# Performance work log

Measured on AMD Instinct MI355X. Metric: run time of the kernel, lower is better.

Reference implementation:

```python
import math
import jax, jax.numpy as jnp
import numpy as np

B, N, D_FULL, M, D_V = 8, 4096, 256, 256, 256


def _phi(x, omega):
    # x: [..., N, d_full], omega: [M, d_full] -> [..., N, M]
    proj = x @ omega.T
    log_phi = proj - 0.5 * jnp.sum(x * x, axis=-1, keepdims=True)
    log_phi = log_phi - jnp.max(log_phi, axis=-1, keepdims=True)
    return jnp.exp(log_phi) / math.sqrt(omega.shape[0])


def _causal(phi_q, phi_k, V):
    # phi_q/phi_k: [B, N, M], V: [B, N, d_v]
    b, n, m = phi_q.shape
    d_v = V.shape[-1]

    def step(carry, inp):
        S, z = carry
        pq, pk, v = inp  # [B,M], [B,M], [B,d_v]
        S = S + pk[:, :, None] * v[:, None, :]          # [B, M, d_v]
        z = z + pk                                       # [B, M]
        num = jnp.einsum('bi,bij->bj', pq, S)            # [B, d_v]
        den = jnp.maximum(jnp.sum(pq * z, axis=-1), 1e-6)
        return (S, z), num / den[:, None]

    S0 = jnp.zeros((b, m, d_v), phi_q.dtype)
    z0 = jnp.zeros((b, m), phi_q.dtype)
    xs = (jnp.swapaxes(phi_q, 0, 1), jnp.swapaxes(phi_k, 0, 1), jnp.swapaxes(V, 0, 1))
    _, ys = jax.lax.scan(step, (S0, z0), xs)  # ys: [N, B, d_v]
    return jnp.swapaxes(ys, 0, 1)


def setup_inputs() -> dict:
    key = jax.random.key(0)
    kq, kk, kv, ko = jax.random.split(key, 4)
    Q = jax.random.normal(kq, (B, N, D_FULL), dtype=jnp.float32)
    K_in = jax.random.normal(kk, (B, N, D_FULL), dtype=jnp.float32)
    V = jax.random.normal(kv, (B, N, D_V), dtype=jnp.float32)
    omega = jax.random.normal(ko, (M, D_FULL), dtype=jnp.float32)
    return {"Q": Q, "K_in": K_in, "V": V, "omega": omega, "causal": 1}


def reference(Q, K_in, V, omega, causal):
    phi_q = _phi(Q, omega)
    phi_k = _phi(K_in, omega)
    if causal:
        return _causal(phi_q, phi_k, V)
    S = jnp.einsum('bni,bnj->bij', phi_k, V)          # [B, M, d_v]
    z = jnp.sum(phi_k, axis=-2)                        # [B, M]
    num = jnp.einsum('bni,bij->bnj', phi_q, S)
    den = jnp.maximum(jnp.einsum('bni,bi->bn', phi_q, z), 1e-6)
    return num / den[..., None]
```

## Files before the change

### kernel.cpp

```cpp
#include <hip/hip_runtime.h>

#define BN 8
#define NN 4096
#define DD 256
#define MM 256
#define DV 256
#define CHUNK 256
#define NC (NN / CHUNK)

using f32x4 = __attribute__((ext_vector_type(4))) float;
using s16x8 = __attribute__((ext_vector_type(8))) short;

#define MFMA16(a, b, c) __builtin_amdgcn_mfma_f32_16x16x32_bf16(a, b, c, 0, 0, 0)


__device__ __forceinline__ unsigned short f2bf(float x) {
    union { float f; unsigned int u; } v; v.f = x;
    unsigned int r = v.u + 0x7FFF + ((v.u >> 16) & 1);
    return (unsigned short)(r >> 16);
}
__device__ __forceinline__ float bf2f(unsigned short u) {
    union { unsigned int u; float f; } v; v.u = ((unsigned int)u) << 16;
    return v.f;
}

__device__ __forceinline__ void split4(const float4 x, unsigned short h[4], unsigned short l[4])
{
    const float xs[4] = {x.x, x.y, x.z, x.w};
#pragma unroll
    for (int j = 0; j < 4; ++j) {
        union { float f; unsigned u; } v; v.f = xs[j];
        const unsigned hm = v.u & 0xFFFF0000u;
        union { unsigned u; float f; } hv; hv.u = hm;
        h[j] = (unsigned short)(hm >> 16);
        l[j] = f2bf(xs[j] - hv.f);
    }
}

__global__ __launch_bounds__(256) void omconv(
    const float* __restrict__ Om, unsigned short* __restrict__ OmH,
    unsigned short* __restrict__ OmL)
{
    const int i = blockIdx.x * 256 + threadIdx.x;
    const int row = i >> 6;
    const int k0  = (i & 63) * 4;
    const float4 v = *(const float4*)(Om + (size_t)row * DD + k0);
    const int wv = row >> 6, ct = (row >> 4) & 3, colL = row & 15;
    const int kt = k0 >> 5, quad = (k0 >> 3) & 3, e0 = k0 & 7;
    const int lanep = quad * 16 + colL;
    const size_t off = ((size_t)((wv * 8 + kt) * 4 + ct) * 64 + lanep) * 8 + e0;
    unsigned short h[4], l[4];
    split4(v, h, l);
    *(uint2*)(OmH + off) = *(uint2*)h;
    *(uint2*)(OmL + off) = *(uint2*)l;
}

__global__ __launch_bounds__(256, 4) void phi_fused(
    const float* __restrict__ Qp, const float* __restrict__ Kp,
    const unsigned short* __restrict__ OmH, const unsigned short* __restrict__ OmL,
    unsigned short* __restrict__ PhiQ, unsigned short* __restrict__ PhiKF,
    unsigned short* __restrict__ PhiTF, float* __restrict__ Zp)
{
    const int tid = threadIdx.x;
    const int w = tid >> 6;
    const int lane = tid & 63;
    const int col = lane & 15, quad = lane >> 4;
    const bool kpath = blockIdx.x < 1024;
    const int id = kpath ? blockIdx.x : (blockIdx.x - 1024);
    const float* __restrict__ X = kpath ? Kp : Qp;
    const long r0 = (long)id * 32;

    __shared__ __align__(16) short AhS[32][264];
    __shared__ __align__(16) short AlS[32][264];
    __shared__ float rowmax_s[32];
    float (*red)[68] = (float(*)[68])AhS;
    unsigned short (*P)[264] = (unsigned short(*)[264])AlS;
    unsigned int* P32 = (unsigned int*)AlS;

    {
        float4 xv[8];
#pragma unroll
        for (int j = 0; j < 8; ++j) {
            const int row = w * 8 + j;
            xv[j] = *(const float4*)(X + (r0 + row) * DD + lane * 4);
        }
#pragma unroll
        for (int j = 0; j < 8; ++j) {
            const int row = w * 8 + j;
            unsigned short h[4], l[4];
            split4(xv[j], h, l);
            *(uint2*)&AhS[row][lane * 4] = *(uint2*)h;
            *(uint2*)&AlS[row][lane * 4] = *(uint2*)l;
        }
    }

    const unsigned short* OmHw = OmH + (size_t)w * 8 * 4 * 512;
    const unsigned short* OmLw = OmL + (size_t)w * 8 * 4 * 512;
    f32x4 acc[2][4] = {};
    s16x8 bh0[4], bl0[4], bh1[4], bl1[4];
#pragma unroll
    for (int ct = 0; ct < 4; ++ct) {
        const size_t off = ((size_t)ct * 64 + lane) * 8;
        bh0[ct] = *(const s16x8*)(OmHw + off);
        bl0[ct] = *(const s16x8*)(OmLw + off);
    }
    __syncthreads();

#pragma unroll
    for (int kt = 0; kt < 8; ++kt) {
        if (kt < 7) {
#pragma unroll
            for (int ct = 0; ct < 4; ++ct) {
                const size_t off = ((size_t)((kt + 1) * 4 + ct) * 64 + lane) * 8;
                bh1[ct] = *(const s16x8*)(OmHw + off);
                bl1[ct] = *(const s16x8*)(OmLw + off);
            }
        }
#pragma unroll
        for (int t = 0; t < 2; ++t) {
            const s16x8 ah = *(const s16x8*)&AhS[t * 16 + col][kt * 32 + quad * 8];
            const s16x8 al = *(const s16x8*)&AlS[t * 16 + col][kt * 32 + quad * 8];
#pragma unroll
            for (int ct = 0; ct < 4; ++ct) {
                acc[t][ct] = MFMA16(ah, bh0[ct], acc[t][ct]);
                acc[t][ct] = MFMA16(ah, bl0[ct], acc[t][ct]);
                acc[t][ct] = MFMA16(al, bh0[ct], acc[t][ct]);
            }
        }
#pragma unroll
        for (int ct = 0; ct < 4; ++ct) { bh0[ct] = bh1[ct]; bl0[ct] = bl1[ct]; }
    }

    __syncthreads();
#pragma unroll
    for (int t = 0; t < 2; ++t)
#pragma unroll
        for (int r = 0; r < 4; ++r) {
            float m = acc[t][0][r];
#pragma unroll
            for (int ct = 1; ct < 4; ++ct) m = fmaxf(m, acc[t][ct][r]);
            red[t * 16 + quad * 4 + r][w * 16 + col] = m;
        }
    __syncthreads();
    {
        const int row = tid >> 3, seg = tid & 7;
        float m = red[row][seg * 8];
#pragma unroll
        for (int j = 1; j < 8; ++j) m = fmaxf(m, red[row][seg * 8 + j]);
        m = fmaxf(m, __shfl_xor(m, 1));
        m = fmaxf(m, __shfl_xor(m, 2));
        m = fmaxf(m, __shfl_xor(m, 4));
        if (seg == 0) rowmax_s[row] = m;
    }
    __syncthreads();

#pragma unroll
    for (int t = 0; t < 2; ++t)
#pragma unroll
        for (int r = 0; r < 4; ++r) {
            const int n = t * 16 + quad * 4 + r;
            const float rm = rowmax_s[n];
#pragma unroll
            for (int ct = 0; ct < 4; ++ct) {
                const float val = __expf(acc[t][ct][r] - rm) * 0.0625f;
                const unsigned u = (unsigned)f2bf(val);
                const unsigned up = (unsigned)__shfl_xor((int)u, 1);
                if ((col & 1) == 0)
                    P32[n * 132 + w * 32 + ct * 8 + (col >> 1)] = u | (up << 16);
            }
        }
    __syncthreads();

    if (!kpath) {
        const int t7 = tid & 7;
        const int nb = tid >> 3;
#pragma unroll
        for (int s = 0; s < 4; ++s)
            *(uint4*)(PhiQ + (r0 + nb) * MM + t7 * 8 + s * 64) =
                *(const uint4*)&P[nb][t7 * 8 + s * 64];
    } else {
        const int b = id >> 7;
        const int ib = id & 127;
        const int c = ib >> 3;
        const size_t bc = ((size_t)(b * NC + c)) << 16;
        const int jt = (ib >> 1) & 3;
        const int half = ib & 1;
        const int ktp = ib & 7;
#pragma unroll
        for (int p = 0; p < 4; ++p) {
            const int msw = p * 4 + (tid >> 6);
            const int ms = msw >> 1, wl = msw & 1;
            const uint4 v = *(const uint4*)&P[wl * 16 + (lane & 15)][ms * 32 + (lane >> 4) * 8];
            *(uint4*)(PhiKF + bc + (((size_t)(jt * 8 + ms) * 4 + half * 2 + wl) * 64 + lane) * 8) = v;
        }
#pragma unroll
        for (int p = 0; p < 4; ++p) {
            const int mq = p, t = tid >> 6;
            unsigned short u[8];
#pragma unroll
            for (int e = 0; e < 8; ++e)
                u[e] = P[(lane >> 4) * 8 + e][mq * 64 + t * 16 + (lane & 15)];
            *(uint4*)(PhiTF + bc + (((size_t)(mq * 8 + ktp) * 4 + t) * 64 + lane) * 8) = *(uint4*)u;
        }
        float z = 0.f;
#pragma unroll
        for (int n = 0; n < 32; ++n) z += bf2f(P[n][tid]);
        atomicAdd(&Zp[((b * NC + c) << 8) + tid], z);
    }
}

__global__ __launch_bounds__(256) void transpose_v(
    const float* __restrict__ V, unsigned short* __restrict__ VTF)
{
    const int tid = threadIdx.x;
    const int ct = blockIdx.x & 3;
    const long r0 = (long)(blockIdx.x >> 2) * 64;
    const int b = (int)(r0 >> 12);
    const int n0 = (int)(r0 & (NN - 1));
    const int c = n0 >> 8;
    const int kt0 = (n0 & 255) >> 5;
    const size_t bc = ((size_t)(b * NC + c)) << 16;
    __shared__ unsigned short T[64][72];
    const int rr = tid >> 4, cs = tid & 15;
#pragma unroll
    for (int p = 0; p < 4; ++p) {
        const int r = p * 16 + rr;
        const float4 v = *(const float4*)(V + (r0 + r) * DV + ct * 64 + cs * 4);
        T[cs * 4 + 0][r] = f2bf(v.x); T[cs * 4 + 1][r] = f2bf(v.y);
        T[cs * 4 + 2][r] = f2bf(v.z); T[cs * 4 + 3][r] = f2bf(v.w);
    }
    __syncthreads();
    const int t = (tid >> 6) & 3, lane = tid & 63;
#pragma unroll
    for (int p = 0; p < 2; ++p) {
        const int kt2 = p;
        const uint4 v = *(const uint4*)&T[t * 16 + (lane & 15)][kt2 * 32 + (lane >> 4) * 8];
        *(uint4*)(VTF + bc + (((size_t)(ct * 8 + kt0 + kt2) * 4 + t) * 64 + lane) * 8) = v;
    }
}

__global__ __launch_bounds__(256, 3) void state_mfma(
    const unsigned short* __restrict__ VTF, const unsigned short* __restrict__ PhiTF,
    unsigned short* __restrict__ STF)
{
    const int tid = threadIdx.x;
    const int w = tid >> 6;
    const int lane = tid & 63;
    const int col = lane & 15, quad = lane >> 4;
    const int q  = blockIdx.x >> 7;
    const int bci = blockIdx.x & 127;
    const int c  = bci & 15;
    const int b  = bci >> 4;
    const int dvq = (q & 1) * 2 + (w & 1);
    const int mq  = (q >> 1) * 2 + (w >> 1);
    const size_t bc = ((size_t)(b * NC + c)) << 16;
    const unsigned short* Af = VTF   + bc + (size_t)dvq * 16384;
    const unsigned short* Bf = PhiTF + bc + (size_t)mq  * 16384;

    f32x4 acc[4][4] = {};
    s16x8 a0[4], b0[4], a1[4], b1[4];
#pragma unroll
    for (int t = 0; t < 4; ++t) {
        a0[t] = *(const s16x8*)(Af + ((size_t)t * 64 + lane) * 8);
        b0[t] = *(const s16x8*)(Bf + ((size_t)t * 64 + lane) * 8);
    }
#pragma unroll
    for (int kt = 0; kt < 8; ++kt) {
        if (kt < 7) {
#pragma unroll
            for (int t = 0; t < 4; ++t) {
                a1[t] = *(const s16x8*)(Af + ((size_t)((kt + 1) * 4 + t) * 64 + lane) * 8);
                b1[t] = *(const s16x8*)(Bf + ((size_t)((kt + 1) * 4 + t) * 64 + lane) * 8);
            }
        }
#pragma unroll
        for (int i = 0; i < 4; ++i)
#pragma unroll
            for (int j = 0; j < 4; ++j) acc[i][j] = MFMA16(b0[i], a0[j], acc[i][j]);
#pragma unroll
        for (int t = 0; t < 4; ++t) { a0[t] = a1[t]; b0[t] = b1[t]; }
    }
#pragma unroll
    for (int i = 0; i < 4; ++i)
#pragma unroll
        for (int j = 0; j < 4; ++j) {
            unsigned short s[4];
#pragma unroll
            for (int r = 0; r < 4; ++r) s[r] = f2bf(acc[i][j][r]);
            const int lanep = ((i & 1) * 2 + (quad >> 1)) * 16 + col;
            const size_t off = (((size_t)(dvq * 8 + mq * 2 + (i >> 1)) * 4 + j) * 64 + lanep) * 8 + (quad & 1) * 4;
            *(uint2*)(STF + bc + off) = *(uint2*)s;
        }
}

__global__ __launch_bounds__(256) void prefix2(
    unsigned short* __restrict__ ST, float* __restrict__ Z)
{
    const long idx = (long)blockIdx.x * 256 + threadIdx.x;
    const int b = (int)(idx >> 16);
    const int r = (int)(idx & 65535);
    float run = 0.f;
#pragma unroll
    for (int c = 0; c < NC; ++c) {
        const size_t off = (((size_t)(b * NC + c)) << 16) + r;
        const float v = bf2f(ST[off]);
        ST[off] = f2bf(run);
        run += v;
    }
    if (idx < BN * MM) {
        const int b2 = (int)(idx >> 8);
        const int m = (int)(idx & 255);
        float rz = 0.f;
#pragma unroll
        for (int c = 0; c < NC; ++c) {
            const size_t off = (size_t)(b2 * NC + c) * MM + m;
            const float v = Z[off];
            Z[off] = rz;
            rz += v;
        }
    }
}

__global__ __launch_bounds__(256) void out_mfma(
    const unsigned short* __restrict__ PhiQ, const unsigned short* __restrict__ PhiKF,
    const unsigned short* __restrict__ VTF, const unsigned short* __restrict__ STF,
    const float* __restrict__ Z, float* __restrict__ Out)
{
    const int tid = threadIdx.x;
    const int w = tid >> 6;
    const int lane = tid & 63;
    const int col = lane & 15, quad = lane >> 4;
    const int it = 3 - (blockIdx.x >> 7);
    const int low = blockIdx.x & 127;
    const int c  = low & 15;
    const int b  = low >> 4;
    const size_t chunk_row = (size_t)b * NN + (size_t)c * CHUNK;
    const size_t bc = ((size_t)(b * NC + c)) << 16;
    const unsigned short* Qrow = PhiQ + (chunk_row + it * 64) * MM;
    const unsigned short* Vf = VTF + bc + (size_t)w * 16384;
    const unsigned short* Sf = STF + bc + (size_t)w * 16384;

    __shared__ unsigned short Qs[64][264];
    __shared__ unsigned short A_s[64][72];
    __shared__ float red[64][68];
    __shared__ float z_s[256];
    __shared__ float den_s[64];

    const float zval = Z[((size_t)(b * NC + c) << 8) + tid];
    s16x8 bk0[8], bk1[8];
#pragma unroll
    for (int ms = 0; ms < 8; ++ms)
        bk0[ms] = *(const s16x8*)(PhiKF + bc + (((size_t)ms * 4 + w) * 64 + lane) * 8);
    uint4 qv[8];
#pragma unroll
    for (int i = 0; i < 8; ++i)
        qv[i] = *((const uint4*)Qrow + i * 256 + tid);
    z_s[tid] = zval;
#pragma unroll
    for (int i = 0; i < 8; ++i) {
        const int f = i * 256 + tid;
        *(uint4*)&Qs[f >> 5][(f & 31) * 8] = qv[i];
    }
    __syncthreads();

    f32x4 oacc[4][4] = {};
    float rsum[4][4] = {};

    for (int jt = 0; jt <= it; ++jt) {
        s16x8 bv[8];
#pragma unroll
        for (int ks2 = 0; ks2 < 2; ++ks2)
#pragma unroll
            for (int t2 = 0; t2 < 4; ++t2)
                bv[ks2 * 4 + t2] = *(const s16x8*)(Vf + (((size_t)(jt * 2 + ks2) * 4 + t2) * 64 + lane) * 8);
        f32x4 accA[4] = {};
#pragma unroll
        for (int ms = 0; ms < 8; ++ms)
#pragma unroll
            for (int t = 0; t < 4; ++t) {
                const s16x8 aq = *(const s16x8*)&Qs[t * 16 + col][ms * 32 + quad * 8];
                accA[t] = MFMA16(aq, bk0[ms], accA[t]);
            }
        if (jt < it) {
#pragma unroll
            for (int ms = 0; ms < 8; ++ms)
                bk1[ms] = *(const s16x8*)(PhiKF + bc + (((size_t)((jt + 1) * 8 + ms) * 4 + w) * 64 + lane) * 8);
        }
        __syncthreads();
#pragma unroll
        for (int t = 0; t < 4; ++t)
#pragma unroll
            for (int r = 0; r < 4; ++r) {
                const int i_loc = t * 16 + quad * 4 + r;
                const int j_loc = w * 16 + col;
                float v = (jt * 64 + j_loc <= it * 64 + i_loc) ? accA[t][r] : 0.f;
                rsum[t][r] += v;
                A_s[i_loc][j_loc] = f2bf(v);
            }
        __syncthreads();
#pragma unroll
        for (int ks2 = 0; ks2 < 2; ++ks2) {
            s16x8 av[4];
#pragma unroll
            for (int t = 0; t < 4; ++t)
                av[t] = *(const s16x8*)&A_s[t * 16 + col][ks2 * 32 + quad * 8];
#pragma unroll
            for (int t2 = 0; t2 < 4; ++t2)
#pragma unroll
                for (int t = 0; t < 4; ++t)
                    oacc[t][t2] = MFMA16(av[t], bv[ks2 * 4 + t2], oacc[t][t2]);
        }
#pragma unroll
        for (int ms = 0; ms < 8; ++ms) bk0[ms] = bk1[ms];
    }
#pragma unroll
    for (int t = 0; t < 4; ++t)
#pragma unroll
        for (int r = 0; r < 4; ++r)
            red[t * 16 + quad * 4 + r][w * 16 + col] = rsum[t][r];

    s16x8 bs0[4], bs1[4];
#pragma unroll
    for (int t2 = 0; t2 < 4; ++t2)
        bs0[t2] = *(const s16x8*)(Sf + ((size_t)t2 * 64 + lane) * 8);
#pragma unroll
    for (int ms = 0; ms < 8; ++ms) {
        if (ms < 7) {
#pragma unroll
            for (int t2 = 0; t2 < 4; ++t2)
                bs1[t2] = *(const s16x8*)(Sf + ((size_t)((ms + 1) * 4 + t2) * 64 + lane) * 8);
        }
        s16x8 aq[4];
#pragma unroll
        for (int t = 0; t < 4; ++t)
            aq[t] = *(const s16x8*)&Qs[t * 16 + col][ms * 32 + quad * 8];
#pragma unroll
        for (int t2 = 0; t2 < 4; ++t2)
#pragma unroll
            for (int t = 0; t < 4; ++t)
                oacc[t][t2] = MFMA16(aq[t], bs0[t2], oacc[t][t2]);
#pragma unroll
        for (int t2 = 0; t2 < 4; ++t2) bs0[t2] = bs1[t2];
    }
    {
        const int i = tid & 63;
        const int seg = tid >> 6;
        float d = 0.f;
#pragma unroll
        for (int g = 0; g < 8; ++g) {
            const s16x8 qv8 = *(const s16x8*)&Qs[i][seg * 64 + g * 8];
#pragma unroll
            for (int x = 0; x < 8; ++x)
                d = fmaf(bf2f((unsigned short)qv8[x]), z_s[seg * 64 + g * 8 + x], d);
        }
        red[i][64 + seg] = d;
    }
    __syncthreads();
    if (tid < 64) {
        float s = 0.f;
#pragma unroll
        for (int j = 0; j < 68; ++j) s += red[tid][j];
        den_s[tid] = fmaxf(s, 1e-6f);
    }
    __syncthreads();
#pragma unroll
    for (int t = 0; t < 4; ++t)
#pragma unroll
        for (int r = 0; r < 4; ++r) {
            const int i_loc = t * 16 + quad * 4 + r;
            const float invd = 1.0f / den_s[i_loc];
#pragma unroll
            for (int t2 = 0; t2 < 4; ++t2)
                Out[(chunk_row + it * 64 + i_loc) * DV + w * 64 + t2 * 16 + col] = oacc[t][t2][r] * invd;
        }
}

extern "C" void kernel_launch(void* const* d_in, const int* in_sizes, int n_in,
                              void* d_out, int out_size, void* d_ws, size_t ws_size,
                              hipStream_t stream)
{
    const float* Q  = (const float*)d_in[0];
    const float* K  = (const float*)d_in[1];
    const float* V  = (const float*)d_in[2];
    const float* Om = (const float*)d_in[3];
    float* out = (float*)d_out;

    const size_t NM = (size_t)BN * NN * MM;
    unsigned short* PhiQ  = (unsigned short*)d_ws;
    unsigned short* PhiKF = PhiQ + NM;
    unsigned short* PhiTF = PhiKF + NM;
    unsigned short* VTF   = PhiTF + NM;
    unsigned short* STF   = VTF + NM;
    unsigned short* OmH   = STF + (size_t)BN * NC * DV * MM;
    unsigned short* OmL   = OmH + (size_t)MM * DD;
    float* Z = (float*)(OmL + (size_t)MM * DD);

    hipMemsetAsync(Z, 0, (size_t)BN * NC * MM * sizeof(float), stream);
    omconv<<<dim3(64), dim3(256), 0, stream>>>(Om, OmH, OmL);
    phi_fused<<<dim3(2048), dim3(256), 0, stream>>>(Q, K, OmH, OmL, PhiQ, PhiKF, PhiTF, Z);
    transpose_v<<<dim3((BN * NN) / 64 * 4), dim3(256), 0, stream>>>(V, VTF);
    state_mfma<<<dim3(BN * NC * 4), dim3(256), 0, stream>>>(VTF, PhiTF, STF);
    prefix2<<<dim3((BN * DV * MM) / 256), dim3(256), 0, stream>>>(STF, Z);
    out_mfma<<<dim3(BN * NC * 4), dim3(256), 0, stream>>>(PhiQ, PhiKF, VTF, STF, Z, out);
}
```

Baseline: 222.1 us.

## Store phiQ in MFMA fragment layout, fuse V transpose into phi kernel

Writes phi_Q directly in the MFMA-fragment layout used for phi_K, so out_mfma loads Q fragments straight from global memory instead of staging a 64x256 tile in LDS. The separate transpose_v launch is folded into phi_fused as extra blocks, removing one kernel launch. The row-sum and denominator reductions now use wave shuffles with a smaller LDS buffer, and the register double-buffering of K and S fragments is dropped in favour of per-iteration loads. The intent is less LDS use and fewer launches, but Q fragments are now re-read from global or L2 on every jt iteration.

Result: no change. 222.4 us (+0.1%).

```diff
diff --git a/kernel.cpp b/kernel.cpp
--- a/kernel.cpp
+++ b/kernel.cpp
@@ -57,18 +57,16 @@
 
 __global__ __launch_bounds__(256, 4) void phi_fused(
     const float* __restrict__ Qp, const float* __restrict__ Kp,
+    const float* __restrict__ Vp,
     const unsigned short* __restrict__ OmH, const unsigned short* __restrict__ OmL,
-    unsigned short* __restrict__ PhiQ, unsigned short* __restrict__ PhiKF,
-    unsigned short* __restrict__ PhiTF, float* __restrict__ Zp)
+    unsigned short* __restrict__ PhiQF, unsigned short* __restrict__ PhiKF,
+    unsigned short* __restrict__ PhiTF, unsigned short* __restrict__ VTF,
+    float* __restrict__ Zp)
 {
     const int tid = threadIdx.x;
     const int w = tid >> 6;
     const int lane = tid & 63;
     const int col = lane & 15, quad = lane >> 4;
-    const bool kpath = blockIdx.x < 1024;
-    const int id = kpath ? blockIdx.x : (blockIdx.x - 1024);
-    const float* __restrict__ X = kpath ? Kp : Qp;
-    const long r0 = (long)id * 32;
 
     __shared__ __align__(16) short AhS[32][264];
     __shared__ __align__(16) short AlS[32][264];
@@ -77,6 +75,39 @@
     unsigned short (*P)[264] = (unsigned short(*)[264])AlS;
     unsigned int* P32 = (unsigned int*)AlS;
 
+    if (blockIdx.x >= 2048) {
+        const int vid = blockIdx.x - 2048;
+        const int ct = vid & 3;
+        const long r0v = (long)(vid >> 2) * 64;
+        const int b = (int)(r0v >> 12);
+        const int n0 = (int)(r0v & (NN - 1));
+        const int c = n0 >> 8;
+        const int kt0 = (n0 & 255) >> 5;
+        const size_t bcv = ((size_t)(b * NC + c)) << 16;
+        unsigned short (*T)[72] = (unsigned short(*)[72])AhS;
+        const int rr = tid >> 4, cs = tid & 15;
+#pragma unroll
+        for (int p = 0; p < 4; ++p) {
+            const int r = p * 16 + rr;
+            const float4 v = *(const float4*)(Vp + (r0v + r) * DV + ct * 64 + cs * 4);
+            T[cs * 4 + 0][r] = f2bf(v.x); T[cs * 4 + 1][r] = f2bf(v.y);
+            T[cs * 4 + 2][r] = f2bf(v.z); T[cs * 4 + 3][r] = f2bf(v.w);
+        }
+        __syncthreads();
+        const int tq = w;
+#pragma unroll
+        for (int p = 0; p < 2; ++p) {
+            const uint4 v = *(const uint4*)&T[tq * 16 + col][p * 32 + quad * 8];
+            *(uint4*)(VTF + bcv + (((size_t)(ct * 8 + kt0 + p) * 4 + tq) * 64 + lane) * 8) = v;
+        }
+        return;
+    }
+
+    const bool kpath = blockIdx.x < 1024;
+    const int id = kpath ? blockIdx.x : (blockIdx.x - 1024);
+    const float* __restrict__ X = kpath ? Kp : Qp;
+    const long r0 = (long)id * 32;
+
     {
         float4 xv[8];
 #pragma unroll
@@ -171,71 +202,37 @@
         }
     __syncthreads();
 
-    if (!kpath) {
-        const int t7 = tid & 7;
-        const int nb = tid >> 3;
-#pragma unroll
-        for (int s = 0; s < 4; ++s)
-            *(uint4*)(PhiQ + (r0 + nb) * MM + t7 * 8 + s * 64) =
-                *(const uint4*)&P[nb][t7 * 8 + s * 64];
-    } else {
+    {
         const int b = id >> 7;
         const int ib = id & 127;
         const int c = ib >> 3;
         const size_t bc = ((size_t)(b * NC + c)) << 16;
         const int jt = (ib >> 1) & 3;
         const int half = ib & 1;
-        const int ktp = ib & 7;
+        unsigned short* __restrict__ PF = kpath ? PhiKF : PhiQF;
 #pragma unroll
         for (int p = 0; p < 4; ++p) {
-            const int msw = p * 4 + (tid >> 6);
+            const int msw = p * 4 + w;
             const int ms = msw >> 1, wl = msw & 1;
-            const uint4 v = *(const uint4*)&P[wl * 16 + (lane & 15)][ms * 32 + (lane >> 4) * 8];
-            *(uint4*)(PhiKF + bc + (((size_t)(jt * 8 + ms) * 4 + half * 2 + wl) * 64 + lane) * 8) = v;
-        }
-#pragma unroll
-        for (int p = 0; p < 4; ++p) {
-            const int mq = p, t = tid >> 6;
-            unsigned short u[8];
-#pragma unroll
-            for (int e = 0; e < 8; ++e)
-                u[e] = P[(lane >> 4) * 8 + e][mq * 64 + t * 16 + (lane & 15)];
-            *(uint4*)(PhiTF + bc + (((size_t)(mq * 8 + ktp) * 4 + t) * 64 + lane) * 8) = *(uint4*)u;
-        }
-        float z = 0.f;
-#pragma unroll
-        for (int n = 0; n < 32; ++n) z += bf2f(P[n][tid]);
-        atomicAdd(&Zp[((b * NC + c) << 8) + tid], z);
-    }
-}
-
-__global__ __launch_bounds__(256) void transpose_v(
-    const float* __restrict__ V, unsigned short* __restrict__ VTF)
-{
-    const int tid = threadIdx.x;
-    const int ct = blockIdx.x & 3;
-    const long r0 = (long)(blockIdx.x >> 2) * 64;
-    const int b = (int)(r0 >> 12);
-    const int n0 = (int)(r0 & (NN - 1));
-    const int c = n0 >> 8;
-    const int kt0 = (n0 & 255) >> 5;
-    const size_t bc = ((size_t)(b * NC + c)) << 16;
-    __shared__ unsigned short T[64][72];
-    const int rr = tid >> 4, cs = tid & 15;
-#pragma unroll
-    for (int p = 0; p < 4; ++p) {
-        const int r = p * 16 + rr;
-        const float4 v = *(const float4*)(V + (r0 + r) * DV + ct * 64 + cs * 4);
-        T[cs * 4 + 0][r] = f2bf(v.x); T[cs * 4 + 1][r] = f2bf(v.y);
-        T[cs * 4 + 2][r] = f2bf(v.z); T[cs * 4 + 3][r] = f2bf(v.w);
-    }
-    __syncthreads();
-    const int t = (tid >> 6) & 3, lane = tid & 63;
-#pragma unroll
-    for (int p = 0; p < 2; ++p) {
-        const int kt2 = p;
-        const uint4 v = *(const uint4*)&T[t * 16 + (lane & 15)][kt2 * 32 + (lane >> 4) * 8];
-        *(uint4*)(VTF + bc + (((size_t)(ct * 8 + kt0 + kt2) * 4 + t) * 64 + lane) * 8) = v;
+            const uint4 v = *(const uint4*)&P[wl * 16 + col][ms * 32 + quad * 8];
+            *(uint4*)(PF + bc + (((size_t)(jt * 8 + ms) * 4 + half * 2 + wl) * 64 + lane) * 8) = v;
+        }
+        if (kpath) {
+            const int ktp = ib & 7;
+#pragma unroll
+            for (int p = 0; p < 4; ++p) {
+                const int mq = p, t = w;
+                unsigned short u[8];
+#pragma unroll
+                for (int e = 0; e < 8; ++e)
+                    u[e] = P[quad * 8 + e][mq * 64 + t * 16 + col];
+                *(uint4*)(PhiTF + bc + (((size_t)(mq * 8 + ktp) * 4 + t) * 64 + lane) * 8) = *(uint4*)u;
+            }
+            float z = 0.f;
+#pragma unroll
+            for (int n = 0; n < 32; ++n) z += bf2f(P[n][tid]);
+            atomicAdd(&Zp[((b * NC + c) << 8) + tid], z);
+        }
     }
 }
 
@@ -322,7 +319,7 @@
 }
 
 __global__ __launch_bounds__(256) void out_mfma(
-    const unsigned short* __restrict__ PhiQ, const unsigned short* __restrict__ PhiKF,
+    const unsigned short* __restrict__ PhiQF, const unsigned short* __restrict__ PhiKF,
     const unsigned short* __restrict__ VTF, const unsigned short* __restrict__ STF,
     const float* __restrict__ Z, float* __restrict__ Out)
 {
@@ -336,55 +333,32 @@
     const int b  = low >> 4;
     const size_t chunk_row = (size_t)b * NN + (size_t)c * CHUNK;
     const size_t bc = ((size_t)(b * NC + c)) << 16;
-    const unsigned short* Qrow = PhiQ + (chunk_row + it * 64) * MM;
+    const unsigned short* Qf = PhiQF + bc + (size_t)it * 16384;
     const unsigned short* Vf = VTF + bc + (size_t)w * 16384;
     const unsigned short* Sf = STF + bc + (size_t)w * 16384;
 
-    __shared__ unsigned short Qs[64][264];
     __shared__ unsigned short A_s[64][72];
-    __shared__ float red[64][68];
+    __shared__ float red[64][20];
     __shared__ float z_s[256];
     __shared__ float den_s[64];
 
-    const float zval = Z[((size_t)(b * NC + c) << 8) + tid];
-    s16x8 bk0[8], bk1[8];
-#pragma unroll
-    for (int ms = 0; ms < 8; ++ms)
-        bk0[ms] = *(const s16x8*)(PhiKF + bc + (((size_t)ms * 4 + w) * 64 + lane) * 8);
-    uint4 qv[8];
-#pragma unroll
-    for (int i = 0; i < 8; ++i)
-        qv[i] = *((const uint4*)Qrow + i * 256 + tid);
-    z_s[tid] = zval;
-#pragma unroll
-    for (int i = 0; i < 8; ++i) {
-        const int f = i * 256 + tid;
-        *(uint4*)&Qs[f >> 5][(f & 31) * 8] = qv[i];
-    }
-    __syncthreads();
+    z_s[tid] = Z[(bc >> 8) + tid];
 
     f32x4 oacc[4][4] = {};
     float rsum[4][4] = {};
 
     for (int jt = 0; jt <= it; ++jt) {
-        s16x8 bv[8];
-#pragma unroll
-        for (int ks2 = 0; ks2 < 2; ++ks2)
-#pragma unroll
-            for (int t2 = 0; t2 < 4; ++t2)
-                bv[ks2 * 4 + t2] = *(const s16x8*)(Vf + (((size_t)(jt * 2 + ks2) * 4 + t2) * 64 + lane) * 8);
         f32x4 accA[4] = {};
 #pragma unroll
-        for (int ms = 0; ms < 8; ++ms)
-#pragma unroll
-            for (int t = 0; t < 4; ++t) {
-                const s16x8 aq = *(const s16x8*)&Qs[t * 16 + col][ms * 32 + quad * 8];
-                accA[t] = MFMA16(aq, bk0[ms], accA[t]);
-            }
-        if (jt < it) {
-#pragma unroll
-            for (int ms = 0; ms < 8; ++ms)
-                bk1[ms] = *(const s16x8*)(PhiKF + bc + (((size_t)((jt + 1) * 8 + ms) * 4 + w) * 64 + lane) * 8);
+        for (int ms = 0; ms < 8; ++ms) {
+            const s16x8 bk = *(const s16x8*)(PhiKF + bc + (((size_t)(jt * 8 + ms) * 4 + w) * 64 + lane) * 8);
+            s16x8 aq[4];
+#pragma unroll
+            for (int t = 0; t < 4; ++t)
+                aq[t] = *(const s16x8*)(Qf + (((size_t)ms * 4 + t) * 64 + lane) * 8);
+#pragma unroll
+            for (int t = 0; t < 4; ++t)
+                accA[t] = MFMA16(aq[t], bk, accA[t]);
         }
         __syncthreads();
 #pragma unroll
@@ -400,6 +374,10 @@
         __syncthreads();
 #pragma unroll
         for (int ks2 = 0; ks2 < 2; ++ks2) {
+            s16x8 bv[4];
+#pragma unroll
+            for (int t2 = 0; t2 < 4; ++t2)
+                bv[t2] = *(const s16x8*)(Vf + (((size_t)(jt * 2 + ks2) * 4 + t2) * 64 + lane) * 8);
             s16x8 av[4];
 #pragma unroll
             for (int t = 0; t < 4; ++t)
@@ -408,58 +386,54 @@
             for (int t2 = 0; t2 < 4; ++t2)
 #pragma unroll
                 for (int t = 0; t < 4; ++t)
-                    oacc[t][t2] = MFMA16(av[t], bv[ks2 * 4 + t2], oacc[t][t2]);
-        }
-#pragma unroll
-        for (int ms = 0; ms < 8; ++ms) bk0[ms] = bk1[ms];
-    }
+                    oacc[t][t2] = MFMA16(av[t], bv[t2], oacc[t][t2]);
+        }
+    }
+
 #pragma unroll
     for (int t = 0; t < 4; ++t)
 #pragma unroll
-        for (int r = 0; r < 4; ++r)
-            red[t * 16 + quad * 4 + r][w * 16 + col] = rsum[t][r];
-
-    s16x8 bs0[4], bs1[4];
-#pragma unroll
-    for (int t2 = 0; t2 < 4; ++t2)
-        bs0[t2] = *(const s16x8*)(Sf + ((size_t)t2 * 64 + lane) * 8);
+        for (int r = 0; r < 4; ++r) {
+            float v = rsum[t][r];
+            v += __shfl_xor(v, 1);
+            v += __shfl_xor(v, 2);
+            v += __shfl_xor(v, 4);
+            v += __shfl_xor(v, 8);
+            if (col == 0) red[t * 16 + quad * 4 + r][w] = v;
+        }
+
+    float dpart[4] = {0.f, 0.f, 0.f, 0.f};
 #pragma unroll
     for (int ms = 0; ms < 8; ++ms) {
-        if (ms < 7) {
-#pragma unroll
-            for (int t2 = 0; t2 < 4; ++t2)
-                bs1[t2] = *(const s16x8*)(Sf + ((size_t)((ms + 1) * 4 + t2) * 64 + lane) * 8);
-        }
-        s16x8 aq[4];
+        s16x8 bs[4], aq[4];
+#pragma unroll
+        for (int t2 = 0; t2 < 4; ++t2)
+            bs[t2] = *(const s16x8*)(Sf + (((size_t)ms * 4 + t2) * 64 + lane) * 8);
 #pragma unroll
         for (int t = 0; t < 4; ++t)
-            aq[t] = *(const s16x8*)&Qs[t * 16 + col][ms * 32 + quad * 8];
+            aq[t] = *(const s16x8*)(Qf + (((size_t)ms * 4 + t) * 64 + lane) * 8);
 #pragma unroll
         for (int t2 = 0; t2 < 4; ++t2)
 #pragma unroll
             for (int t = 0; t < 4; ++t)
-                oacc[t][t2] = MFMA16(aq[t], bs0[t2], oacc[t][t2]);
-#pragma unroll
-        for (int t2 = 0; t2 < 4; ++t2) bs0[t2] = bs1[t2];
-    }
-    {
-        const int i = tid & 63;
-        const int seg = tid >> 6;
-        float d = 0.f;
-#pragma unroll
-        for (int g = 0; g < 8; ++g) {
-            const s16x8 qv8 = *(const s16x8*)&Qs[i][seg * 64 + g * 8];
-#pragma unroll
-            for (int x = 0; x < 8; ++x)
-                d = fmaf(bf2f((unsigned short)qv8[x]), z_s[seg * 64 + g * 8 + x], d);
-        }
-        red[i][64 + seg] = d;
-    }
+                oacc[t][t2] = MFMA16(aq[t], bs[t2], oacc[t][t2]);
+        if ((ms >> 1) == w) {
+#pragma unroll
+            for (int t = 0; t < 4; ++t)
+#pragma unroll
+                for (int e = 0; e < 8; ++e)
+                    dpart[t] = fmaf(bf2f((unsigned short)aq[t][e]),
+                                    z_s[ms * 32 + quad * 8 + e], dpart[t]);
+        }
+    }
+#pragma unroll
+    for (int t = 0; t < 4; ++t)
+        red[t * 16 + col][4 + w * 4 + quad] = dpart[t];
     __syncthreads();
     if (tid < 64) {
         float s = 0.f;
 #pragma unroll
-        for (int j = 0; j < 68; ++j) s += red[tid][j];
+        for (int j = 0; j < 20; ++j) s += red[tid][j];
         den_s[tid] = fmaxf(s, 1e-6f);
     }
     __syncthreads();
@@ -486,8 +460,8 @@
     float* out = (float*)d_out;
 
     const size_t NM = (size_t)BN * NN * MM;
-    unsigned short* PhiQ  = (unsigned short*)d_ws;
-    unsigned short* PhiKF = PhiQ + NM;
+    unsigned short* PhiQF = (unsigned short*)d_ws;
+    unsigned short* PhiKF = PhiQF + NM;
     unsigned short* PhiTF = PhiKF + NM;
     unsigned short* VTF   = PhiTF + NM;
     unsigned short* STF   = VTF + NM;
@@ -497,9 +471,8 @@
 
     hipMemsetAsync(Z, 0, (size_t)BN * NC * MM * sizeof(float), stream);
     omconv<<<dim3(64), dim3(256), 0, stream>>>(Om, OmH, OmL);
-    phi_fused<<<dim3(2048), dim3(256), 0, stream>>>(Q, K, OmH, OmL, PhiQ, PhiKF, PhiTF, Z);
-    transpose_v<<<dim3((BN * NN) / 64 * 4), dim3(256), 0, stream>>>(V, VTF);
+    phi_fused<<<dim3(4096), dim3(256), 0, stream>>>(Q, K, V, OmH, OmL, PhiQF, PhiKF, PhiTF, VTF, Z);
     state_mfma<<<dim3(BN * NC * 4), dim3(256), 0, stream>>>(VTF, PhiTF, STF);
     prefix2<<<dim3((BN * DV * MM) / 256), dim3(256), 0, stream>>>(STF, Z);
-    out_mfma<<<dim3(BN * NC * 4), dim3(256), 0, stream>>>(PhiQ, PhiKF, VTF, STF, Z, out);
-}
+    out_mfma<<<dim3(BN * NC * 4), dim3(256), 0, stream>>>(PhiQF, PhiKF, VTF, STF, Z, out);
+}
```
